# Performance work log

Measured on AMD Instinct MI355X. Metric: run time of the kernel, lower is better.

Reference implementation:

```python
import jax, jax.numpy as jnp
import numpy as np

N = 100000   # nodes
E = 1600000  # edges
F = 128      # input node features
H = 128      # hidden channels
G = 512      # graphs in batch
EPS = 1e-5   # BatchNorm eps


def setup_inputs() -> dict:
    key = jax.random.key(0)
    ks = jax.random.split(key, 24)
    x = jax.random.normal(ks[0], (N, F), jnp.float32)
    edge_index = jax.random.randint(ks[1], (2, E), 0, N)
    batch = jnp.sort(jax.random.randint(ks[2], (N,), 0, G))

    def lin_w(k, i, o):
        return jax.random.normal(k, (i, o), jnp.float32) / np.sqrt(i)

    inp = {
        "x": x, "edge_index": edge_index, "batch": batch,
        "W1": lin_w(ks[3], F, H), "b1": jnp.zeros((H,), jnp.float32),
        "g1": jnp.ones((H,), jnp.float32), "be1": jnp.zeros((H,), jnp.float32),
        "m1": 0.1 * jax.random.normal(ks[4], (H,), jnp.float32),
        "v1": jax.random.uniform(ks[5], (H,), jnp.float32) + 0.5,
        "W2": lin_w(ks[6], H, H), "b2": jnp.zeros((H,), jnp.float32),
        "g2": jnp.ones((H,), jnp.float32), "be2": jnp.zeros((H,), jnp.float32),
        "m2": 0.1 * jax.random.normal(ks[7], (H,), jnp.float32),
        "v2": jax.random.uniform(ks[8], (H,), jnp.float32) + 0.5,
        "W3": lin_w(ks[9], H, H), "b3": jnp.zeros((H,), jnp.float32),
        "g3": jnp.ones((H,), jnp.float32), "be3": jnp.zeros((H,), jnp.float32),
        "m3": 0.1 * jax.random.normal(ks[10], (H,), jnp.float32),
        "v3": jax.random.uniform(ks[11], (H,), jnp.float32) + 0.5,
        "Wl": lin_w(ks[12], H, 1), "bl": jnp.zeros((1,), jnp.float32),
    }
    return inp


def _gcn_norm(edge_index):
    # add self-loops, then symmetric normalization deg^-1/2 A_hat deg^-1/2
    loops = jnp.arange(N)
    src = jnp.concatenate([edge_index[0], loops])
    dst = jnp.concatenate([edge_index[1], loops])
    deg = jax.ops.segment_sum(jnp.ones_like(src, jnp.float32), dst, num_segments=N)
    dinv = jax.lax.rsqrt(jnp.maximum(deg, 1.0))
    norm = dinv[src] * dinv[dst]  # [E+N]
    return src, dst, norm


def _gcn_conv(x, W, b, src, dst, norm):
    h = x @ W                                    # [N,H] dense GEMM first (PyG order)
    msg = h[src] * norm[:, None]                 # gather + scale, [E+N,H]
    agg = jax.ops.segment_sum(msg, dst, num_segments=N)  # scatter-add
    return agg + b


def _bn_relu(x, g, be, m, v):
    # inference BatchNorm1d (running stats) + ReLU
    return jax.nn.relu((x - m) * jax.lax.rsqrt(v + EPS) * g + be)


def reference(x, edge_index, batch,
              W1, b1, g1, be1, m1, v1,
              W2, b2, g2, be2, m2, v2,
              W3, b3, g3, be3, m3, v3,
              Wl, bl):
    src, dst, norm = _gcn_norm(edge_index)
    h = _bn_relu(_gcn_conv(x, W1, b1, src, dst, norm), g1, be1, m1, v1)
    h = _bn_relu(_gcn_conv(h, W2, b2, src, dst, norm), g2, be2, m2, v2)
    h = _bn_relu(_gcn_conv(h, W3, b3, src, dst, norm), g3, be3, m3, v3)
    # global mean pool over graphs
    sums = jax.ops.segment_sum(h, batch, num_segments=G)           # [G,H]
    cnt = jax.ops.segment_sum(jnp.ones((N,), jnp.float32), batch, num_segments=G)
    pooled = sums / jnp.maximum(cnt, 1.0)[:, None]
    # dropout is identity at inference; final linear
    return pooled @ Wl + bl  # [G,1]
```

## Files before the change

kernel.cpp:

```cpp
#include <hip/hip_runtime.h>
#include <hip/hip_bf16.h>

#define NN 100000
#define NE 1600000
#define HD 128
#define NG 512
#define BN_EPS 1e-5f
#define NXCD 8

#define GEMM_BLOCKS 1563
#define HIST_BLOCKS 6250

typedef __attribute__((ext_vector_type(8))) short short8;
typedef __attribute__((ext_vector_type(4))) float floatx4;

__device__ __forceinline__ ushort f2bf(float f) {
    union { float f; uint u; } v; v.f = f;
    uint r = (v.u + 0x7FFF + ((v.u >> 16) & 1)) >> 16;
    return (ushort)r;
}
__device__ __forceinline__ float bflo(uint u) { union { uint u; float f; } v; v.u = u << 16; return v.f; }
__device__ __forceinline__ float bfhi(uint u) { union { uint u; float f; } v; v.u = u & 0xFFFF0000u; return v.f; }

__device__ __forceinline__ uint xcc_id() {
    return (uint)__builtin_amdgcn_s_getreg(20 | (31 << 11)) & (NXCD - 1);
}

__global__ void k_zero_i(int* p, int n) {
    int i = blockIdx.x * 256 + threadIdx.x;
    if (i < n) p[i] = 0;
}

__global__ void k_prep_w3(const float* __restrict__ W1, const float* __restrict__ W2,
                          const float* __restrict__ W3,
                          ushort* __restrict__ Wt1, ushort* __restrict__ Wt2,
                          ushort* __restrict__ Wt3) {
    int w = blockIdx.x >> 6;
    int i = (blockIdx.x & 63) * 256 + threadIdx.x;
    const float* W = (w == 0) ? W1 : (w == 1) ? W2 : W3;
    ushort* Wt = (w == 0) ? Wt1 : (w == 1) ? Wt2 : Wt3;
    int k = i >> 7, n = i & 127;
    Wt[n * 128 + k] = f2bf(W[i]);
}

__launch_bounds__(256)
__global__ void k_fused1(const float* __restrict__ x, const ushort* __restrict__ Wt,
                         ushort* __restrict__ hs,
                         const int* __restrict__ dst, int* __restrict__ indeg,
                         int* __restrict__ rank) {
    const int tid = threadIdx.x;
    if (blockIdx.x >= GEMM_BLOCKS) {
        int e = (blockIdx.x - GEMM_BLOCKS) * 256 + tid;
        if (e < NE) {
            uint xc = xcc_id();
            int d = dst[e];
            int lr = __hip_atomic_fetch_add(&indeg[xc * NN + d], 1,
                                            __ATOMIC_RELAXED, __HIP_MEMORY_SCOPE_WORKGROUP);
            rank[e] = (int)((xc << 24) | (uint)lr);
        }
        return;
    }
    const int wave = tid >> 6, lane = tid & 63;
    const int m = lane & 15, kg = lane >> 4;
    const long row0 = (long)blockIdx.x * 64 + wave * 16;

    long arow = row0 + m;
    long arc = arow < NN ? arow : (NN - 1);
    const float* xf = x + arc * 128;
    short8 a[4];
#pragma unroll
    for (int s = 0; s < 4; ++s) {
        float4 f0 = *(const float4*)(xf + s * 32 + kg * 8);
        float4 f1 = *(const float4*)(xf + s * 32 + kg * 8 + 4);
        short8 t;
        t[0] = (short)f2bf(f0.x); t[1] = (short)f2bf(f0.y);
        t[2] = (short)f2bf(f0.z); t[3] = (short)f2bf(f0.w);
        t[4] = (short)f2bf(f1.x); t[5] = (short)f2bf(f1.y);
        t[6] = (short)f2bf(f1.z); t[7] = (short)f2bf(f1.w);
        a[s] = t;
    }

    floatx4 acc[8];
#pragma unroll
    for (int ct = 0; ct < 8; ++ct) acc[ct] = (floatx4){0.f, 0.f, 0.f, 0.f};

#pragma unroll
    for (int s = 0; s < 4; ++s) {
#pragma unroll
        for (int ct = 0; ct < 8; ++ct) {
            short8 b = *(const short8*)(Wt + (ct * 16 + m) * 128 + s * 32 + kg * 8);
            acc[ct] = __builtin_amdgcn_mfma_f32_16x16x32_bf16(a[s], b, acc[ct], 0, 0, 0);
        }
    }

#pragma unroll
    for (int r = 0; r < 4; ++r) {
        long orow = row0 + kg * 4 + r;
        if (orow < NN) {
#pragma unroll
            for (int ct = 0; ct < 8; ++ct)
                hs[orow * 128 + ct * 16 + m] = f2bf(acc[ct][r]);
        }
    }
}

__global__ void k_scan1d(const int* __restrict__ indeg, int* __restrict__ rs,
                         int* __restrict__ aux, float* __restrict__ dinv) {
    __shared__ int s[256];
    int t = threadIdx.x;
    int base = blockIdx.x * 1024 + t * 4;
    int v0 = 0, v1 = 0, v2 = 0, v3 = 0;
#pragma unroll
    for (int xc = 0; xc < NXCD; ++xc) {
        const int* p = indeg + xc * NN;
        if (base + 0 < NN) v0 += p[base + 0];
        if (base + 1 < NN) v1 += p[base + 1];
        if (base + 2 < NN) v2 += p[base + 2];
        if (base + 3 < NN) v3 += p[base + 3];
    }
    if (base + 0 < NN) dinv[base + 0] = rsqrtf((float)(v0 + 1));
    if (base + 1 < NN) dinv[base + 1] = rsqrtf((float)(v1 + 1));
    if (base + 2 < NN) dinv[base + 2] = rsqrtf((float)(v2 + 1));
    if (base + 3 < NN) dinv[base + 3] = rsqrtf((float)(v3 + 1));
    int tsum = v0 + v1 + v2 + v3;
    s[t] = tsum;
    __syncthreads();
    for (int o = 1; o < 256; o <<= 1) {
        int x = 0;
        if (t >= o) x = s[t - o];
        __syncthreads();
        s[t] += x;
        __syncthreads();
    }
    int excl = s[t] - tsum;
    if (base + 0 < NN) rs[base + 0] = excl;
    if (base + 1 < NN) rs[base + 1] = excl + v0;
    if (base + 2 < NN) rs[base + 2] = excl + v0 + v1;
    if (base + 3 < NN) rs[base + 3] = excl + v0 + v1 + v2;
    if (t == 255) aux[blockIdx.x] = s[255];
}

__global__ void k_scan2(int* __restrict__ aux, int nblk) {
    __shared__ int s[128];
    int t = threadIdx.x;
    int v = (t < nblk) ? aux[t] : 0;
    s[t] = v;
    __syncthreads();
    for (int o = 1; o < 128; o <<= 1) {
        int x = 0;
        if (t >= o) x = s[t - o];
        __syncthreads();
        s[t] += x;
        __syncthreads();
    }
    if (t < nblk) aux[t] = s[t] - v;
}

__global__ void k_scan3(int* __restrict__ rs, const int* __restrict__ aux,
                        int* __restrict__ indeg) {
    int i = blockIdx.x * 256 + threadIdx.x;
    if (i < NN) {
        int b = rs[i] + aux[i >> 10];
        rs[i] = b;
        int run = b;
#pragma unroll
        for (int xc = 0; xc < NXCD; ++xc) {
            int c = indeg[xc * NN + i];
            indeg[xc * NN + i] = run;
            run += c;
        }
    }
    if (i == 0) rs[NN] = NE;
}

__global__ void k_fill(const int* __restrict__ src, const int* __restrict__ dst,
                       const int* __restrict__ rank, const int* __restrict__ indeg,
                       int* __restrict__ csr) {
    int e = blockIdx.x * 256 + threadIdx.x;
    if (e >= NE) return;
    uint r = (uint)rank[e];
    int xc = (int)(r >> 24);
    int lr = (int)(r & 0xFFFFFFu);
    csr[indeg[xc * NN + dst[e]] + lr] = src[e];
}

__global__ void k_bn_prep3(const float* __restrict__ b1, const float* __restrict__ g1,
                           const float* __restrict__ be1, const float* __restrict__ m1,
                           const float* __restrict__ v1,
                           const float* __restrict__ b2, const float* __restrict__ g2,
                           const float* __restrict__ be2, const float* __restrict__ m2,
                           const float* __restrict__ v2,
                           const float* __restrict__ b3, const float* __restrict__ g3,
                           const float* __restrict__ be3, const float* __restrict__ m3,
                           const float* __restrict__ v3,
                           float* scale1, float* shift1, float* scale2, float* shift2,
                           float* scale3, float* shift3) {
    int l = blockIdx.x, f = threadIdx.x;
    const float *b, *g, *be, *m, *v;
    float *sc, *sh;
    if (l == 0)      { b = b1; g = g1; be = be1; m = m1; v = v1; sc = scale1; sh = shift1; }
    else if (l == 1) { b = b2; g = g2; be = be2; m = m2; v = v2; sc = scale2; sh = shift2; }
    else             { b = b3; g = g3; be = be3; m = m3; v = v3; sc = scale3; sh = shift3; }
    float s = g[f] * rsqrtf(v[f] + BN_EPS);
    sc[f] = s;
    sh[f] = (b[f] - m[f]) * s + be[f];
}

__global__ void k_gstart(const int* __restrict__ batch, int* __restrict__ gstart) {
    int g = blockIdx.x * 256 + threadIdx.x;
    if (g > NG) return;
    if (g == NG) { gstart[NG] = NN; return; }
    int lo = 0, hi = NN;
    while (lo < hi) {
        int mid = (lo + hi) >> 1;
        if (batch[mid] < g) lo = mid + 1; else hi = mid;
    }
    gstart[g] = lo;
}

#define WT_STRIDE 136
__launch_bounds__(256)
__global__ void k_gemm_l23(const ushort* __restrict__ xb, const ushort* __restrict__ Wt,
                           const float* __restrict__ dinv, ushort* __restrict__ hs) {
    __shared__ ushort sWt[128 * WT_STRIDE];
    const int tid = threadIdx.x;
    for (int i = tid; i < 2048; i += 256) {
        int row = i >> 4, seg = i & 15;
        *(uint4*)&sWt[row * WT_STRIDE + seg * 8] = *(const uint4*)(Wt + row * 128 + seg * 8);
    }
    __syncthreads();

    const int wave = tid >> 6, lane = tid & 63;
    const int m = lane & 15, kg = lane >> 4;
    const long row0 = (long)blockIdx.x * 64 + wave * 16;

    long arow = row0 + m;
    long arc = arow < NN ? arow : (NN - 1);
    short8 a[4];
#pragma unroll
    for (int s = 0; s < 4; ++s)
        a[s] = *(const short8*)(xb + arc * 128 + s * 32 + kg * 8);

    floatx4 acc[8];
#pragma unroll
    for (int ct = 0; ct < 8; ++ct) acc[ct] = (floatx4){0.f, 0.f, 0.f, 0.f};

#pragma unroll
    for (int s = 0; s < 4; ++s) {
#pragma unroll
        for (int ct = 0; ct < 8; ++ct) {
            short8 b = *(const short8*)&sWt[(ct * 16 + m) * WT_STRIDE + s * 32 + kg * 8];
            acc[ct] = __builtin_amdgcn_mfma_f32_16x16x32_bf16(a[s], b, acc[ct], 0, 0, 0);
        }
    }

#pragma unroll
    for (int r = 0; r < 4; ++r) {
        long orow = row0 + kg * 4 + r;
        if (orow < NN) {
            float dd = dinv[orow];
#pragma unroll
            for (int ct = 0; ct < 8; ++ct)
                hs[orow * 128 + ct * 16 + m] = f2bf(acc[ct][r] * dd);
        }
    }
}

template <bool SCALE_SRC>
__launch_bounds__(256)
__global__ void k_gather_w(const ushort* __restrict__ hs, const int* __restrict__ rs,
                           const int* __restrict__ csr, const float* __restrict__ dinv,
                           const float* __restrict__ scale, const float* __restrict__ shift,
                           ushort* __restrict__ xout) {
    const int tid = threadIdx.x;
    const int d = blockIdx.x * 4 + (tid >> 6);
    const int lane = tid & 63;
    const int sub = lane >> 4;
    const int c0 = (lane & 15) * 8;

    const int e0 = rs[d], e1 = rs[d + 1];
    const float dd = dinv[d];

    float a0 = 0.f, a1 = 0.f, a2 = 0.f, a3 = 0.f,
          a4 = 0.f, a5 = 0.f, a6 = 0.f, a7 = 0.f;

    if (sub == 0) {
        uint4 sv = *(const uint4*)(hs + (long)d * 128 + c0);
        float w = SCALE_SRC ? dd : 1.0f;
        a0 = w * bflo(sv.x); a1 = w * bfhi(sv.x);
        a2 = w * bflo(sv.y); a3 = w * bfhi(sv.y);
        a4 = w * bflo(sv.z); a5 = w * bfhi(sv.z);
        a6 = w * bflo(sv.w); a7 = w * bfhi(sv.w);
    }

    int j = e0 + sub;
    int s0 = 0, s1 = 0;
    bool have = (j < e1 - 4);
    if (have) { s0 = csr[j]; s1 = csr[j + 4]; }
    while (have) {
        int jn = j + 8;
        bool nxt = (jn < e1 - 4);
        int n0 = 0, n1 = 0;
        if (nxt) { n0 = csr[jn]; n1 = csr[jn + 4]; }
        float w0 = SCALE_SRC ? dinv[s0] : 1.0f;
        float w1 = SCALE_SRC ? dinv[s1] : 1.0f;
        uint4 v0 = *(const uint4*)(hs + (long)s0 * 128 + c0);
        uint4 v1 = *(const uint4*)(hs + (long)s1 * 128 + c0);
        a0 += w0 * bflo(v0.x) + w1 * bflo(v1.x);
        a1 += w0 * bfhi(v0.x) + w1 * bfhi(v1.x);
        a2 += w0 * bflo(v0.y) + w1 * bflo(v1.y);
        a3 += w0 * bfhi(v0.y) + w1 * bfhi(v1.y);
        a4 += w0 * bflo(v0.z) + w1 * bflo(v1.z);
        a5 += w0 * bfhi(v0.z) + w1 * bfhi(v1.z);
        a6 += w0 * bflo(v0.w) + w1 * bflo(v1.w);
        a7 += w0 * bfhi(v0.w) + w1 * bfhi(v1.w);
        j = jn; s0 = n0; s1 = n1; have = nxt;
    }
    if (j < e1) {
        int sx = csr[j];
        float wx = SCALE_SRC ? dinv[sx] : 1.0f;
        uint4 v0 = *(const uint4*)(hs + (long)sx * 128 + c0);
        a0 += wx * bflo(v0.x); a1 += wx * bfhi(v0.x);
        a2 += wx * bflo(v0.y); a3 += wx * bfhi(v0.y);
        a4 += wx * bflo(v0.z); a5 += wx * bfhi(v0.z);
        a6 += wx * bflo(v0.w); a7 += wx * bfhi(v0.w);
    }

    a0 += __shfl_xor(a0, 16); a1 += __shfl_xor(a1, 16);
    a2 += __shfl_xor(a2, 16); a3 += __shfl_xor(a3, 16);
    a4 += __shfl_xor(a4, 16); a5 += __shfl_xor(a5, 16);
    a6 += __shfl_xor(a6, 16); a7 += __shfl_xor(a7, 16);
    a0 += __shfl_xor(a0, 32); a1 += __shfl_xor(a1, 32);
    a2 += __shfl_xor(a2, 32); a3 += __shfl_xor(a3, 32);
    a4 += __shfl_xor(a4, 32); a5 += __shfl_xor(a5, 32);
    a6 += __shfl_xor(a6, 32); a7 += __shfl_xor(a7, 32);

    if (sub == 0) {
        float4 sca = *(const float4*)(scale + c0);
        float4 scb = *(const float4*)(scale + c0 + 4);
        float4 sha = *(const float4*)(shift + c0);
        float4 shb = *(const float4*)(shift + c0 + 4);
        float r0 = fmaxf(dd * a0 * sca.x + sha.x, 0.f);
        float r1 = fmaxf(dd * a1 * sca.y + sha.y, 0.f);
        float r2 = fmaxf(dd * a2 * sca.z + sha.z, 0.f);
        float r3 = fmaxf(dd * a3 * sca.w + sha.w, 0.f);
        float r4 = fmaxf(dd * a4 * scb.x + shb.x, 0.f);
        float r5 = fmaxf(dd * a5 * scb.y + shb.y, 0.f);
        float r6 = fmaxf(dd * a6 * scb.z + shb.z, 0.f);
        float r7 = fmaxf(dd * a7 * scb.w + shb.w, 0.f);
        uint4 o;
        o.x = (uint)f2bf(r0) | ((uint)f2bf(r1) << 16);
        o.y = (uint)f2bf(r2) | ((uint)f2bf(r3) << 16);
        o.z = (uint)f2bf(r4) | ((uint)f2bf(r5) << 16);
        o.w = (uint)f2bf(r6) | ((uint)f2bf(r7) << 16);
        *(uint4*)(xout + (long)d * 128 + c0) = o;
    }
}

__global__ void k_pool_final2(const ushort* __restrict__ x, const int* __restrict__ gstart,
                              const float* __restrict__ Wl, const float* __restrict__ bl,
                              float* __restrict__ out) {
    __shared__ float red[256];
    int g = blockIdx.x;
    int tid = threadIdx.x;
    int f = tid & 127;
    int half = tid >> 7;
    int i0 = gstart[g], i1 = gstart[g + 1];

    float acc = 0.f;
    for (int i = i0 + half; i < i1; i += 2) {
        union { uint u; float f; } v; v.u = (uint)x[(long)i * 128 + f] << 16;
        acc += v.f;
    }
    red[tid] = acc;
    __syncthreads();
    if (tid < 128) red[tid] = (red[tid] + red[tid + 128]) * Wl[tid];
    __syncthreads();
    for (int o = 64; o > 0; o >>= 1) {
        if (tid < o) red[tid] += red[tid + o];
        __syncthreads();
    }
    if (tid == 0) out[g] = red[0] / fmaxf((float)(i1 - i0), 1.f) + bl[0];
}

extern "C" void kernel_launch(void* const* d_in, const int* in_sizes, int n_in,
                              void* d_out, int out_size, void* d_ws, size_t ws_size,
                              hipStream_t stream) {
    const float* x   = (const float*)d_in[0];
    const int*   ei  = (const int*)d_in[1];
    const int*   bat = (const int*)d_in[2];
    const float* W1  = (const float*)d_in[3];
    const float* b1  = (const float*)d_in[4];
    const float* g1  = (const float*)d_in[5];
    const float* be1 = (const float*)d_in[6];
    const float* m1  = (const float*)d_in[7];
    const float* v1  = (const float*)d_in[8];
    const float* W2  = (const float*)d_in[9];
    const float* b2  = (const float*)d_in[10];
    const float* g2  = (const float*)d_in[11];
    const float* be2 = (const float*)d_in[12];
    const float* m2  = (const float*)d_in[13];
    const float* v2  = (const float*)d_in[14];
    const float* W3  = (const float*)d_in[15];
    const float* b3  = (const float*)d_in[16];
    const float* g3  = (const float*)d_in[17];
    const float* be3 = (const float*)d_in[18];
    const float* m3  = (const float*)d_in[19];
    const float* v3  = (const float*)d_in[20];
    const float* Wl  = (const float*)d_in[21];
    const float* bl  = (const float*)d_in[22];
    float* out = (float*)d_out;

    const int* srcp = ei;
    const int* dstp = ei + NE;

    char* ws = (char*)d_ws;
    size_t off = 0;
    auto alloc = [&](size_t bytes) { char* p = ws + off; off += (bytes + 255) & ~255ULL; return p; };
    float*  dinv   = (float*) alloc(NN * 4);
    int*    indeg  = (int*)   alloc((size_t)NXCD * NN * 4);
    int*    rs     = (int*)   alloc((NN + 1) * 4);
    int*    aux    = (int*)   alloc(128 * 4);
    int*    csr    = (int*)   alloc(NE * 4);
    int*    rank   = (int*)   alloc(NE * 4);
    float*  scale1 = (float*) alloc(HD * 4);
    float*  shift1 = (float*) alloc(HD * 4);
    float*  scale2 = (float*) alloc(HD * 4);
    float*  shift2 = (float*) alloc(HD * 4);
    float*  scale3 = (float*) alloc(HD * 4);
    float*  shift3 = (float*) alloc(HD * 4);
    int*    gstart = (int*)   alloc((NG + 1) * 4);
    ushort* Wt1    = (ushort*)alloc(128 * 128 * 2);
    ushort* Wt2    = (ushort*)alloc(128 * 128 * 2);
    ushort* Wt3    = (ushort*)alloc(128 * 128 * 2);
    ushort* hs     = (ushort*)alloc((size_t)NN * HD * 2);
    ushort* xbuf   = (ushort*)alloc((size_t)NN * HD * 2);

    const int nblk_scan = (NN + 1023) / 1024;
    const int grid_n    = (NN + 255) / 256;
    const int grid_e    = (NE + 255) / 256;
    const int gath_grid = NN / 4;

    k_zero_i<<<(NXCD * NN + 255) / 256, 256, 0, stream>>>(indeg, NXCD * NN);
    k_prep_w3<<<192, 256, 0, stream>>>(W1, W2, W3, Wt1, Wt2, Wt3);

    k_fused1<<<GEMM_BLOCKS + HIST_BLOCKS, 256, 0, stream>>>(x, Wt1, hs, dstp, indeg, rank);

    k_scan1d<<<nblk_scan, 256, 0, stream>>>(indeg, rs, aux, dinv);
    k_scan2<<<1, 128, 0, stream>>>(aux, nblk_scan);
    k_scan3<<<grid_n, 256, 0, stream>>>(rs, aux, indeg);
    k_fill<<<grid_e, 256, 0, stream>>>(srcp, dstp, rank, indeg, csr);

    k_bn_prep3<<<3, 128, 0, stream>>>(b1, g1, be1, m1, v1, b2, g2, be2, m2, v2,
                                      b3, g3, be3, m3, v3,
                                      scale1, shift1, scale2, shift2, scale3, shift3);
    k_gstart<<<3, 256, 0, stream>>>(bat, gstart);

    k_gather_w<true><<<gath_grid, 256, 0, stream>>>(hs, rs, csr, dinv, scale1, shift1, xbuf);
    k_gemm_l23<<<GEMM_BLOCKS, 256, 0, stream>>>(xbuf, Wt2, dinv, hs);
    k_gather_w<false><<<gath_grid, 256, 0, stream>>>(hs, rs, csr, dinv, scale2, shift2, xbuf);
    k_gemm_l23<<<GEMM_BLOCKS, 256, 0, stream>>>(xbuf, Wt3, dinv, hs);
    k_gather_w<false><<<gath_grid, 256, 0, stream>>>(hs, rs, csr, dinv, scale3, shift3, xbuf);

    k_pool_final2<<<NG, 256, 0, stream>>>(xbuf, gstart, Wl, bl, out);
}
```

Measured before the change: 524.8 us.

## Build CSR via two-level binned counting sort and fuse pooling into last gather

Replaces the per-XCD global-atomic degree histogram, three-pass scan and fill with a two-level binned sort. It builds per-block bin histograms in shared memory, runs a single-block bin scan, scatters packed src/low-dst words into bins, and then builds each bin's CSR slice with shared-memory atomics. The last gather layer now folds the final linear projection into its epilogue and atomically accumulates per-graph partial sums, which removes the third xbuf write and the separate pool kernel. The small prep kernels are merged into one launch. Edge order within a CSR row becomes nondeterministic, and the float atomics in pooling make the reduction order vary between runs.

```diff
diff --git a/kernel.cpp b/kernel.cpp
--- a/kernel.cpp
+++ b/kernel.cpp
@@ -6,10 +6,13 @@
 #define HD 128
 #define NG 512
 #define BN_EPS 1e-5f
-#define NXCD 8
 
 #define GEMM_BLOCKS 1563
-#define HIST_BLOCKS 6250
+
+#define BIN_SHIFT 8
+#define NBIN 391
+#define TILE 16384
+#define NBLK_BIN 98
 
 typedef __attribute__((ext_vector_type(8))) short short8;
 typedef __attribute__((ext_vector_type(4))) float floatx4;
@@ -22,42 +25,76 @@
 __device__ __forceinline__ float bflo(uint u) { union { uint u; float f; } v; v.u = u << 16; return v.f; }
 __device__ __forceinline__ float bfhi(uint u) { union { uint u; float f; } v; v.u = u & 0xFFFF0000u; return v.f; }
 
-__device__ __forceinline__ uint xcc_id() {
-    return (uint)__builtin_amdgcn_s_getreg(20 | (31 << 11)) & (NXCD - 1);
-}
-
-__global__ void k_zero_i(int* p, int n) {
-    int i = blockIdx.x * 256 + threadIdx.x;
-    if (i < n) p[i] = 0;
-}
-
-__global__ void k_prep_w3(const float* __restrict__ W1, const float* __restrict__ W2,
-                          const float* __restrict__ W3,
-                          ushort* __restrict__ Wt1, ushort* __restrict__ Wt2,
-                          ushort* __restrict__ Wt3) {
-    int w = blockIdx.x >> 6;
-    int i = (blockIdx.x & 63) * 256 + threadIdx.x;
-    const float* W = (w == 0) ? W1 : (w == 1) ? W2 : W3;
-    ushort* Wt = (w == 0) ? Wt1 : (w == 1) ? Wt2 : Wt3;
-    int k = i >> 7, n = i & 127;
-    Wt[n * 128 + k] = f2bf(W[i]);
+__global__ void k_prep_all(const float* __restrict__ W1, const float* __restrict__ W2,
+                           const float* __restrict__ W3,
+                           ushort* __restrict__ Wt1, ushort* __restrict__ Wt2,
+                           ushort* __restrict__ Wt3,
+                           const float* __restrict__ b1, const float* __restrict__ g1,
+                           const float* __restrict__ be1, const float* __restrict__ m1,
+                           const float* __restrict__ v1,
+                           const float* __restrict__ b2, const float* __restrict__ g2,
+                           const float* __restrict__ be2, const float* __restrict__ m2,
+                           const float* __restrict__ v2,
+                           const float* __restrict__ b3, const float* __restrict__ g3,
+                           const float* __restrict__ be3, const float* __restrict__ m3,
+                           const float* __restrict__ v3,
+                           float* scale1, float* shift1, float* scale2, float* shift2,
+                           float* scale3, float* shift3,
+                           const int* __restrict__ bat, float* __restrict__ invcnt,
+                           float* __restrict__ out2d) {
+    int blk = blockIdx.x, tid = threadIdx.x;
+    if (blk < 192) {
+        int w = blk >> 6;
+        int i = (blk & 63) * 256 + tid;
+        const float* W = (w == 0) ? W1 : (w == 1) ? W2 : W3;
+        ushort* Wt = (w == 0) ? Wt1 : (w == 1) ? Wt2 : Wt3;
+        int k = i >> 7, n = i & 127;
+        Wt[n * 128 + k] = f2bf(W[i]);
+    } else if (blk < 195) {
+        if (tid < 128) {
+            int l = blk - 192;
+            const float *b, *g, *be, *m, *v;
+            float *sc, *sh;
+            if (l == 0)      { b = b1; g = g1; be = be1; m = m1; v = v1; sc = scale1; sh = shift1; }
+            else if (l == 1) { b = b2; g = g2; be = be2; m = m2; v = v2; sc = scale2; sh = shift2; }
+            else             { b = b3; g = g3; be = be3; m = m3; v = v3; sc = scale3; sh = shift3; }
+            float s = g[tid] * rsqrtf(v[tid] + BN_EPS);
+            sc[tid] = s;
+            sh[tid] = (b[tid] - m[tid]) * s + be[tid];
+        }
+    } else {
+        int g = (blk - 195) * 256 + tid;
+        if (g < NG) {
+            int lo = 0, hi = NN;
+            while (lo < hi) { int mid = (lo + hi) >> 1; if (bat[mid] < g) lo = mid + 1; else hi = mid; }
+            int lo2 = lo, hi2 = NN;
+            while (lo2 < hi2) { int mid = (lo2 + hi2) >> 1; if (bat[mid] < g + 1) lo2 = mid + 1; else hi2 = mid; }
+            int cnt = lo2 - lo;
+            invcnt[g] = 1.f / fmaxf((float)cnt, 1.f);
+#pragma unroll
+            for (int i = 0; i < 8; ++i) out2d[g * 8 + i] = 0.f;
+        }
+    }
 }
 
 __launch_bounds__(256)
 __global__ void k_fused1(const float* __restrict__ x, const ushort* __restrict__ Wt,
                          ushort* __restrict__ hs,
-                         const int* __restrict__ dst, int* __restrict__ indeg,
-                         int* __restrict__ rank) {
+                         const int* __restrict__ dst, int* __restrict__ L) {
+    __shared__ int lh[NBIN];
     const int tid = threadIdx.x;
     if (blockIdx.x >= GEMM_BLOCKS) {
-        int e = (blockIdx.x - GEMM_BLOCKS) * 256 + tid;
-        if (e < NE) {
-            uint xc = xcc_id();
-            int d = dst[e];
-            int lr = __hip_atomic_fetch_add(&indeg[xc * NN + d], 1,
-                                            __ATOMIC_RELAXED, __HIP_MEMORY_SCOPE_WORKGROUP);
-            rank[e] = (int)((xc << 24) | (uint)lr);
-        }
+        int blk = blockIdx.x - GEMM_BLOCKS;
+        for (int i = tid; i < NBIN; i += 256) lh[i] = 0;
+        __syncthreads();
+        long base = (long)blk * TILE;
+#pragma unroll 4
+        for (int i = 0; i < TILE / 256; ++i) {
+            long e = base + i * 256 + tid;
+            if (e < NE) atomicAdd(&lh[dst[e] >> BIN_SHIFT], 1);
+        }
+        __syncthreads();
+        for (int i = tid; i < NBIN; i += 256) L[i * NBLK_BIN + blk] = lh[i];
         return;
     }
     const int wave = tid >> 6, lane = tid & 63;
@@ -104,118 +141,90 @@
     }
 }
 
-__global__ void k_scan1d(const int* __restrict__ indeg, int* __restrict__ rs,
-                         int* __restrict__ aux, float* __restrict__ dinv) {
-    __shared__ int s[256];
+__global__ void k_binscan(int* __restrict__ L, int* __restrict__ bin_ebase,
+                          int* __restrict__ rs) {
+    __shared__ int s[512];
     int t = threadIdx.x;
-    int base = blockIdx.x * 1024 + t * 4;
-    int v0 = 0, v1 = 0, v2 = 0, v3 = 0;
-#pragma unroll
-    for (int xc = 0; xc < NXCD; ++xc) {
-        const int* p = indeg + xc * NN;
-        if (base + 0 < NN) v0 += p[base + 0];
-        if (base + 1 < NN) v1 += p[base + 1];
-        if (base + 2 < NN) v2 += p[base + 2];
-        if (base + 3 < NN) v3 += p[base + 3];
-    }
-    if (base + 0 < NN) dinv[base + 0] = rsqrtf((float)(v0 + 1));
-    if (base + 1 < NN) dinv[base + 1] = rsqrtf((float)(v1 + 1));
-    if (base + 2 < NN) dinv[base + 2] = rsqrtf((float)(v2 + 1));
-    if (base + 3 < NN) dinv[base + 3] = rsqrtf((float)(v3 + 1));
-    int tsum = v0 + v1 + v2 + v3;
-    s[t] = tsum;
+    int tot = 0;
+    if (t < NBIN) {
+        int run = 0;
+        for (int b = 0; b < NBLK_BIN; ++b) {
+            int h = L[t * NBLK_BIN + b];
+            L[t * NBLK_BIN + b] = run;
+            run += h;
+        }
+        tot = run;
+    }
+    s[t] = tot;
+    __syncthreads();
+    for (int o = 1; o < 512; o <<= 1) {
+        int x = (t >= o) ? s[t - o] : 0;
+        __syncthreads();
+        s[t] += x;
+        __syncthreads();
+    }
+    int excl = s[t] - tot;
+    if (t < NBIN) {
+        bin_ebase[t] = excl;
+        for (int b = 0; b < NBLK_BIN; ++b) L[t * NBLK_BIN + b] += excl;
+    }
+    if (t == 0) { bin_ebase[NBIN] = NE; rs[NN] = NE; }
+}
+
+__launch_bounds__(256)
+__global__ void k_binscatter(const int* __restrict__ src, const int* __restrict__ dst,
+                             const int* __restrict__ L, uint* __restrict__ bpack) {
+    __shared__ int off[NBIN];
+    int t = threadIdx.x, blk = blockIdx.x;
+    for (int i = t; i < NBIN; i += 256) off[i] = L[i * NBLK_BIN + blk];
+    __syncthreads();
+    long base = (long)blk * TILE;
+#pragma unroll 4
+    for (int i = 0; i < TILE / 256; ++i) {
+        long e = base + i * 256 + t;
+        if (e < NE) {
+            int d = dst[e];
+            int p = atomicAdd(&off[d >> BIN_SHIFT], 1);
+            bpack[p] = (uint)src[e] | ((uint)(d & 255) << 24);
+        }
+    }
+}
+
+__launch_bounds__(256)
+__global__ void k_bincsr(const uint* __restrict__ bpack, const int* __restrict__ bin_ebase,
+                         int* __restrict__ rs, float* __restrict__ dinv,
+                         int* __restrict__ csr) {
+    __shared__ int cnt[256];
+    __shared__ int sc[256];
+    __shared__ int run[256];
+    int t = threadIdx.x, b = blockIdx.x;
+    int e0 = bin_ebase[b], e1 = bin_ebase[b + 1];
+    cnt[t] = 0;
+    __syncthreads();
+    for (int e = e0 + t; e < e1; e += 256) atomicAdd(&cnt[bpack[e] >> 24], 1);
+    __syncthreads();
+    int c = cnt[t];
+    sc[t] = c;
     __syncthreads();
     for (int o = 1; o < 256; o <<= 1) {
-        int x = 0;
-        if (t >= o) x = s[t - o];
-        __syncthreads();
-        s[t] += x;
-        __syncthreads();
-    }
-    int excl = s[t] - tsum;
-    if (base + 0 < NN) rs[base + 0] = excl;
-    if (base + 1 < NN) rs[base + 1] = excl + v0;
-    if (base + 2 < NN) rs[base + 2] = excl + v0 + v1;
-    if (base + 3 < NN) rs[base + 3] = excl + v0 + v1 + v2;
-    if (t == 255) aux[blockIdx.x] = s[255];
-}
-
-__global__ void k_scan2(int* __restrict__ aux, int nblk) {
-    __shared__ int s[128];
-    int t = threadIdx.x;
-    int v = (t < nblk) ? aux[t] : 0;
-    s[t] = v;
-    __syncthreads();
-    for (int o = 1; o < 128; o <<= 1) {
-        int x = 0;
-        if (t >= o) x = s[t - o];
-        __syncthreads();
-        s[t] += x;
-        __syncthreads();
-    }
-    if (t < nblk) aux[t] = s[t] - v;
-}
-
-__global__ void k_scan3(int* __restrict__ rs, const int* __restrict__ aux,
-                        int* __restrict__ indeg) {
-    int i = blockIdx.x * 256 + threadIdx.x;
-    if (i < NN) {
-        int b = rs[i] + aux[i >> 10];
-        rs[i] = b;
-        int run = b;
-#pragma unroll
-        for (int xc = 0; xc < NXCD; ++xc) {
-            int c = indeg[xc * NN + i];
-            indeg[xc * NN + i] = run;
-            run += c;
-        }
-    }
-    if (i == 0) rs[NN] = NE;
-}
-
-__global__ void k_fill(const int* __restrict__ src, const int* __restrict__ dst,
-                       const int* __restrict__ rank, const int* __restrict__ indeg,
-                       int* __restrict__ csr) {
-    int e = blockIdx.x * 256 + threadIdx.x;
-    if (e >= NE) return;
-    uint r = (uint)rank[e];
-    int xc = (int)(r >> 24);
-    int lr = (int)(r & 0xFFFFFFu);
-    csr[indeg[xc * NN + dst[e]] + lr] = src[e];
-}
-
-__global__ void k_bn_prep3(const float* __restrict__ b1, const float* __restrict__ g1,
-                           const float* __restrict__ be1, const float* __restrict__ m1,
-                           const float* __restrict__ v1,
-                           const float* __restrict__ b2, const float* __restrict__ g2,
-                           const float* __restrict__ be2, const float* __restrict__ m2,
-                           const float* __restrict__ v2,
-                           const float* __restrict__ b3, const float* __restrict__ g3,
-                           const float* __restrict__ be3, const float* __restrict__ m3,
-                           const float* __restrict__ v3,
-                           float* scale1, float* shift1, float* scale2, float* shift2,
-                           float* scale3, float* shift3) {
-    int l = blockIdx.x, f = threadIdx.x;
-    const float *b, *g, *be, *m, *v;
-    float *sc, *sh;
-    if (l == 0)      { b = b1; g = g1; be = be1; m = m1; v = v1; sc = scale1; sh = shift1; }
-    else if (l == 1) { b = b2; g = g2; be = be2; m = m2; v = v2; sc = scale2; sh = shift2; }
-    else             { b = b3; g = g3; be = be3; m = m3; v = v3; sc = scale3; sh = shift3; }
-    float s = g[f] * rsqrtf(v[f] + BN_EPS);
-    sc[f] = s;
-    sh[f] = (b[f] - m[f]) * s + be[f];
-}
-
-__global__ void k_gstart(const int* __restrict__ batch, int* __restrict__ gstart) {
-    int g = blockIdx.x * 256 + threadIdx.x;
-    if (g > NG) return;
-    if (g == NG) { gstart[NG] = NN; return; }
-    int lo = 0, hi = NN;
-    while (lo < hi) {
-        int mid = (lo + hi) >> 1;
-        if (batch[mid] < g) lo = mid + 1; else hi = mid;
-    }
-    gstart[g] = lo;
+        int x = (t >= o) ? sc[t - o] : 0;
+        __syncthreads();
+        sc[t] += x;
+        __syncthreads();
+    }
+    int excl = sc[t] - c;
+    int node = (b << BIN_SHIFT) + t;
+    if (node < NN) {
+        rs[node] = e0 + excl;
+        dinv[node] = rsqrtf((float)(c + 1));
+    }
+    run[t] = e0 + excl;
+    __syncthreads();
+    for (int e = e0 + t; e < e1; e += 256) {
+        uint u = bpack[e];
+        int p = atomicAdd(&run[u >> 24], 1);
+        csr[p] = (int)(u & 0xFFFFFFu);
+    }
 }
 
 #define WT_STRIDE 136
@@ -266,12 +275,14 @@
     }
 }
 
-template <bool SCALE_SRC>
+template <bool SCALE_SRC, bool POOL>
 __launch_bounds__(256)
 __global__ void k_gather_w(const ushort* __restrict__ hs, const int* __restrict__ rs,
                            const int* __restrict__ csr, const float* __restrict__ dinv,
                            const float* __restrict__ scale, const float* __restrict__ shift,
-                           ushort* __restrict__ xout) {
+                           ushort* __restrict__ xout,
+                           const int* __restrict__ bat, const float* __restrict__ invcnt,
+                           const float* __restrict__ Wl, float* __restrict__ out2d) {
     const int tid = threadIdx.x;
     const int d = blockIdx.x * 4 + (tid >> 6);
     const int lane = tid & 63;
@@ -335,6 +346,7 @@
     a4 += __shfl_xor(a4, 32); a5 += __shfl_xor(a5, 32);
     a6 += __shfl_xor(a6, 32); a7 += __shfl_xor(a7, 32);
 
+    float pd = 0.f;
     if (sub == 0) {
         float4 sca = *(const float4*)(scale + c0);
         float4 scb = *(const float4*)(scale + c0 + 4);
@@ -348,39 +360,40 @@
         float r5 = fmaxf(dd * a5 * scb.y + shb.y, 0.f);
         float r6 = fmaxf(dd * a6 * scb.z + shb.z, 0.f);
         float r7 = fmaxf(dd * a7 * scb.w + shb.w, 0.f);
-        uint4 o;
-        o.x = (uint)f2bf(r0) | ((uint)f2bf(r1) << 16);
-        o.y = (uint)f2bf(r2) | ((uint)f2bf(r3) << 16);
-        o.z = (uint)f2bf(r4) | ((uint)f2bf(r5) << 16);
-        o.w = (uint)f2bf(r6) | ((uint)f2bf(r7) << 16);
-        *(uint4*)(xout + (long)d * 128 + c0) = o;
-    }
-}
-
-__global__ void k_pool_final2(const ushort* __restrict__ x, const int* __restrict__ gstart,
-                              const float* __restrict__ Wl, const float* __restrict__ bl,
-                              float* __restrict__ out) {
-    __shared__ float red[256];
-    int g = blockIdx.x;
-    int tid = threadIdx.x;
-    int f = tid & 127;
-    int half = tid >> 7;
-    int i0 = gstart[g], i1 = gstart[g + 1];
-
-    float acc = 0.f;
-    for (int i = i0 + half; i < i1; i += 2) {
-        union { uint u; float f; } v; v.u = (uint)x[(long)i * 128 + f] << 16;
-        acc += v.f;
-    }
-    red[tid] = acc;
-    __syncthreads();
-    if (tid < 128) red[tid] = (red[tid] + red[tid + 128]) * Wl[tid];
-    __syncthreads();
-    for (int o = 64; o > 0; o >>= 1) {
-        if (tid < o) red[tid] += red[tid + o];
-        __syncthreads();
-    }
-    if (tid == 0) out[g] = red[0] / fmaxf((float)(i1 - i0), 1.f) + bl[0];
+        if constexpr (POOL) {
+            float4 wa = *(const float4*)(Wl + c0);
+            float4 wb = *(const float4*)(Wl + c0 + 4);
+            pd = r0 * wa.x + r1 * wa.y + r2 * wa.z + r3 * wa.w +
+                 r4 * wb.x + r5 * wb.y + r6 * wb.z + r7 * wb.w;
+        } else {
+            uint4 o;
+            o.x = (uint)f2bf(r0) | ((uint)f2bf(r1) << 16);
+            o.y = (uint)f2bf(r2) | ((uint)f2bf(r3) << 16);
+            o.z = (uint)f2bf(r4) | ((uint)f2bf(r5) << 16);
+            o.w = (uint)f2bf(r6) | ((uint)f2bf(r7) << 16);
+            *(uint4*)(xout + (long)d * 128 + c0) = o;
+        }
+    }
+    if constexpr (POOL) {
+        pd += __shfl_xor(pd, 1);
+        pd += __shfl_xor(pd, 2);
+        pd += __shfl_xor(pd, 4);
+        pd += __shfl_xor(pd, 8);
+        if (lane == 0) {
+            int g = bat[d];
+            atomicAdd(&out2d[g * 8 + (d & 7)], pd * invcnt[g]);
+        }
+    }
+}
+
+__global__ void k_final(const float* __restrict__ out2d, const float* __restrict__ bl,
+                        float* __restrict__ out) {
+    int g = blockIdx.x * 256 + threadIdx.x;
+    if (g >= NG) return;
+    float s = bl[0];
+#pragma unroll
+    for (int i = 0; i < 8; ++i) s += out2d[g * 8 + i];
+    out[g] = s;
 }
 
 extern "C" void kernel_launch(void* const* d_in, const int* in_sizes, int n_in,
@@ -417,50 +430,48 @@
     char* ws = (char*)d_ws;
     size_t off = 0;
     auto alloc = [&](size_t bytes) { char* p = ws + off; off += (bytes + 255) & ~255ULL; return p; };
-    float*  dinv   = (float*) alloc(NN * 4);
-    int*    indeg  = (int*)   alloc((size_t)NXCD * NN * 4);
-    int*    rs     = (int*)   alloc((NN + 1) * 4);
-    int*    aux    = (int*)   alloc(128 * 4);
-    int*    csr    = (int*)   alloc(NE * 4);
-    int*    rank   = (int*)   alloc(NE * 4);
+    float*  dinv     = (float*) alloc(NN * 4);
+    int*    rs       = (int*)   alloc((NN + 1) * 4);
+    int*    L        = (int*)   alloc((size_t)NBIN * NBLK_BIN * 4);
+    int*    bin_ebase= (int*)   alloc((NBIN + 1) * 4);
+    uint*   bpack    = (uint*)  alloc((size_t)NE * 4);
+    int*    csr      = (int*)   alloc((size_t)NE * 4);
     float*  scale1 = (float*) alloc(HD * 4);
     float*  shift1 = (float*) alloc(HD * 4);
     float*  scale2 = (float*) alloc(HD * 4);
     float*  shift2 = (float*) alloc(HD * 4);
     float*  scale3 = (float*) alloc(HD * 4);
     float*  shift3 = (float*) alloc(HD * 4);
-    int*    gstart = (int*)   alloc((NG + 1) * 4);
+    float*  invcnt = (float*) alloc(NG * 4);
+    float*  out2d  = (float*) alloc(NG * 8 * 4);
     ushort* Wt1    = (ushort*)alloc(128 * 128 * 2);
     ushort* Wt2    = (ushort*)alloc(128 * 128 * 2);
     ushort* Wt3    = (ushort*)alloc(128 * 128 * 2);
     ushort* hs     = (ushort*)alloc((size_t)NN * HD * 2);
     ushort* xbuf   = (ushort*)alloc((size_t)NN * HD * 2);
 
-    const int nblk_scan = (NN + 1023) / 1024;
-    const int grid_n    = (NN + 255) / 256;
-    const int grid_e    = (NE + 255) / 256;
     const int gath_grid = NN / 4;
 
-    k_zero_i<<<(NXCD * NN + 255) / 256, 256, 0, stream>>>(indeg, NXCD * NN);
-    k_prep_w3<<<192, 256, 0, stream>>>(W1, W2, W3, Wt1, Wt2, Wt3);
-
-    k_fused1<<<GEMM_BLOCKS + HIST_BLOCKS, 256, 0, stream>>>(x, Wt1, hs, dstp, indeg, rank);
-
-    k_scan1d<<<nblk_scan, 256, 0, stream>>>(indeg, rs, aux, dinv);
-    k_scan2<<<1, 128, 0, stream>>>(aux, nblk_scan);
-    k_scan3<<<grid_n, 256, 0, stream>>>(rs, aux, indeg);
-    k_fill<<<grid_e, 256, 0, stream>>>(srcp, dstp, rank, indeg, csr);
-
-    k_bn_prep3<<<3, 128, 0, stream>>>(b1, g1, be1, m1, v1, b2, g2, be2, m2, v2,
-                                      b3, g3, be3, m3, v3,
-                                      scale1, shift1, scale2, shift2, scale3, shift3);
-    k_gstart<<<3, 256, 0, stream>>>(bat, gstart);
-
-    k_gather_w<true><<<gath_grid, 256, 0, stream>>>(hs, rs, csr, dinv, scale1, shift1, xbuf);
+    k_prep_all<<<197, 256, 0, stream>>>(W1, W2, W3, Wt1, Wt2, Wt3,
+                                        b1, g1, be1, m1, v1, b2, g2, be2, m2, v2,
+                                        b3, g3, be3, m3, v3,
+                                        scale1, shift1, scale2, shift2, scale3, shift3,
+                                        bat, invcnt, out2d);
+
+    k_fused1<<<GEMM_BLOCKS + NBLK_BIN, 256, 0, stream>>>(x, Wt1, hs, dstp, L);
+
+    k_binscan<<<1, 512, 0, stream>>>(L, bin_ebase, rs);
+    k_binscatter<<<NBLK_BIN, 256, 0, stream>>>(srcp, dstp, L, bpack);
+    k_bincsr<<<NBIN, 256, 0, stream>>>(bpack, bin_ebase, rs, dinv, csr);
+
+    k_gather_w<true, false><<<gath_grid, 256, 0, stream>>>(
+        hs, rs, csr, dinv, scale1, shift1, xbuf, nullptr, nullptr, nullptr, nullptr);
     k_gemm_l23<<<GEMM_BLOCKS, 256, 0, stream>>>(xbuf, Wt2, dinv, hs);
-    k_gather_w<false><<<gath_grid, 256, 0, stream>>>(hs, rs, csr, dinv, scale2, shift2, xbuf);
+    k_gather_w<false, false><<<gath_grid, 256, 0, stream>>>(
+        hs, rs, csr, dinv, scale2, shift2, xbuf, nullptr, nullptr, nullptr, nullptr);
     k_gemm_l23<<<GEMM_BLOCKS, 256, 0, stream>>>(xbuf, Wt3, dinv, hs);
-    k_gather_w<false><<<gath_grid, 256, 0, stream>>>(hs, rs, csr, dinv, scale3, shift3, xbuf);
-
-    k_pool_final2<<<NG, 256, 0, stream>>>(xbuf, gstart, Wl, bl, out);
-}
+    k_gather_w<false, true><<<gath_grid, 256, 0, stream>>>(
+        hs, rs, csr, dinv, scale3, shift3, nullptr, bat, invcnt, Wl, out2d);
+
+    k_final<<<2, 256, 0, stream>>>(out2d, bl, out);
+}
```

Result: faster. 505.6 us (-3.7%).
